# Kernel optimization log

Hardware: AMD Instinct MI355X
Metric: run time of the kernel (lower is better)

## Reference

```python
import jax, jax.numpy as jnp
import numpy as np

B, N, F, H, D, HID = 32, 256, 8, 8, 8, 512  # batch, stocks, features, heads, head_dim, hidden
NEG_SLOPE = 0.2
NEG_INF = -1e30


def setup_inputs() -> dict:
    key = jax.random.key(0)
    ks = jax.random.split(key, 20)
    feat = jax.random.normal(ks[0], (B, F, N), jnp.float32)
    adjs = [(jax.random.uniform(ks[1 + i], (B, N, N)) < 0.05).astype(jnp.float32) for i in range(3)]
    inputs = jnp.concatenate(adjs + [feat], axis=1)  # (B, 3N+F, N)
    s = 0.02  # xavier-ish gain used in the torch init
    stdv = 1.0 / np.sqrt(H * D)
    return {
        'inputs': inputs,
        'W_gat': jax.random.normal(ks[4], (3, HID, H * D), jnp.float32) * stdv,
        'Wu': jax.random.normal(ks[5], (3, H, D, 1), jnp.float32),
        'Wv': jax.random.normal(ks[6], (3, H, D, 1), jnp.float32),
        'b_gat': jax.random.normal(ks[7], (3, H * D), jnp.float32) * stdv,
        'projW': jax.random.normal(ks[8], (3, HID, H * D), jnp.float32) * s,
        'projB': jnp.zeros((3, H * D), jnp.float32),
        'w_self1': jax.random.normal(ks[9], (F, HID), jnp.float32) * s,
        'b_self1': jnp.zeros((HID,), jnp.float32),
        'w_mlp': jax.random.normal(ks[10], (3, H * D, HID), jnp.float32) * s,
        'b_mlp': jnp.zeros((3, HID), jnp.float32),
        'w_self2': jax.random.normal(ks[11], (HID, HID), jnp.float32) * s,
        'b_self2': jnp.zeros((HID,), jnp.float32),
        'sem_w1': jax.random.normal(ks[12], (HID, HID), jnp.float32) * s,
        'sem_b1': jnp.zeros((HID,), jnp.float32),
        'sem_w2': jax.random.normal(ks[13], (HID, 1), jnp.float32) * s,
        'gen_w': jax.random.normal(ks[14], (N * HID, N), jnp.float32) * s,
        'gen_b': jnp.zeros((N,), jnp.float32),
    }


def _mhgat(x, adj, W, Wu, Wv, b, pW, pB):
    # x: (B,N,HID), adj: (B,N,N)
    # rows of adj that are entirely zero are replaced by 1e-6 everywhere
    adj = jnp.where(jnp.all(adj == 0, axis=-1, keepdims=True), 1e-6, adj)
    sup = (x @ W).reshape(B, N, H, D).transpose(0, 2, 1, 3)  # (B,H,N,D)
    f1 = jnp.einsum('bhnd,hd->bhn', sup, Wu[..., 0])[:, :, None, :]  # (B,H,1,N)
    f2 = jnp.einsum('bhnd,hd->bhn', sup, Wv[..., 0])[:, :, :, None]  # (B,H,N,1)
    w = jax.nn.leaky_relu(f1 + f2, NEG_SLOPE)  # (B,H,N,N)
    mw = jnp.einsum('bhij,bjk->bhik', w, adj)  # matmul masking, as in torch source
    mask = mw != 0
    # torch.sparse.softmax: softmax over nonzero entries only, zeros elsewhere
    attn = jax.nn.softmax(jnp.where(mask, mw, NEG_INF), axis=3)
    attn = jnp.where(mask, attn, 0.0)
    out = (attn @ sup).transpose(0, 2, 1, 3).reshape(B, N, H * D) + b
    out = out + x @ pW + pB  # residual projection
    return jnp.tanh(out)


def reference(inputs, W_gat, Wu, Wv, b_gat, projW, projB, w_self1, b_self1,
              w_mlp, b_mlp, w_self2, b_self2, sem_w1, sem_b1, sem_w2, gen_w, gen_b):
    ind_adj = inputs[:, :N, :]
    pos_adj = inputs[:, N:2 * N, :]
    neg_adj = inputs[:, 2 * N:3 * N, :]
    x = inputs[:, 3 * N:, :].transpose(0, 2, 1)  # (B,N,F)
    support = x @ w_self1 + b_self1  # (B,N,HID)
    gat_out = [_mhgat(support, a, W_gat[i], Wu[i], Wv[i], b_gat[i], projW[i], projB[i])
               for i, a in enumerate([ind_adj, pos_adj, neg_adj])]
    ind_s, pos_s, neg_s = gat_out
    s2 = support @ w_self2 + b_self2
    ind_o = ind_s @ w_mlp[0] + b_mlp[0]
    pos_o = neg_s @ w_mlp[1] + b_mlp[1]  # NOTE: bug in original source preserved (uses neg_support)
    neg_o = neg_s @ w_mlp[2] + b_mlp[2]
    emb = jnp.stack([s2, ind_o, pos_o, neg_o], axis=1)  # (B,4,N,HID)
    # semantic fusion attention
    wsem = jnp.tanh(emb @ sem_w1 + sem_b1) @ sem_w2  # (B,4,N,1)
    beta = jax.nn.softmax(wsem, axis=1)
    fused = (beta * emb).sum(axis=1)  # (B,N,HID)
    # PairNorm PN-SI, scale=1
    xc = fused - fused.mean(axis=1, keepdims=True)
    xc = xc / jnp.sqrt(1e-6 + (xc ** 2).sum(axis=2, keepdims=True))
    # generator
    flat = xc.reshape(B, N * HID)
    return jax.nn.sigmoid(flat @ gen_w + gen_b)  # (B,N)
```

## Files before the change

### kernel.cpp

```cpp
#include <hip/hip_runtime.h>
#include <math.h>

#define Bk   32
#define Nk   256
#define Fk   8
#define Hk   8
#define Dk   8
#define HIDk 512
#define HDk  64
#define NROWk 776
#define CAPk 96

typedef __attribute__((ext_vector_type(8))) short short8;
typedef __attribute__((ext_vector_type(4))) float f32x4;

__device__ __forceinline__ float lrelu(float x){ return fmaxf(x, 0.2f*x); }

__device__ __forceinline__ unsigned short f2bf(float x){
  unsigned int u = __float_as_uint(x);
  unsigned int r = (u + 0x7fffu + ((u>>16)&1u)) >> 16;
  return (unsigned short)r;
}

__global__ void k_support(const float* __restrict__ inp, const float* __restrict__ w1,
                          const float* __restrict__ b1, float* __restrict__ support){
  int bn = blockIdx.x; int b = bn >> 8; int n = bn & 255;
  const float* xin = inp + (size_t)b*NROWk*Nk + (size_t)(3*Nk)*Nk + n;
  float x[8];
#pragma unroll
  for (int f=0; f<8; f++) x[f] = xin[(size_t)f*Nk];
  int t = threadIdx.x;
  for (int c = t; c < HIDk; c += 256){
    float s = b1[c];
#pragma unroll
    for (int f=0; f<8; f++) s += x[f]*w1[f*HIDk + c];
    support[(size_t)bn*HIDk + c] = s;
  }
}

__global__ void k_sup(const float* __restrict__ support, const float* __restrict__ W,
                      float* __restrict__ sup){
  __shared__ float srow[4][HIDk+1];
  int b = blockIdx.x >> 6; int n0 = (blockIdx.x & 63) << 2;
  int t = threadIdx.x;
  for (int i = t; i < 4*HIDk; i += 256)
    srow[i>>9][i&511] = support[((size_t)b*Nk + n0 + (i>>9))*HIDk + (i&511)];
  __syncthreads();
  int nl = t >> 6, hd = t & 63;
  const float* srw = srow[nl];
  float s = 0.f;
  for (int c=0;c<HIDk;c++) s += srw[c]*W[c*HDk + hd];
  int h = hd >> 3, d = hd & 7;
  sup[(((size_t)b*Hk + h)*Nk + (n0+nl))*Dk + d] = s;
}

__global__ void k_fuv(const float* __restrict__ sup, const float* __restrict__ Wu,
                      const float* __restrict__ Wv, float* __restrict__ fu, float* __restrict__ fv){
  int i = blockIdx.x*256 + threadIdx.x;
  int h = (i >> 8) & 7;
  const float* s = sup + (size_t)i*Dk;
  float a=0.f, v=0.f;
#pragma unroll
  for (int d=0; d<8; d++){ float sv = s[d]; a += sv*Wu[h*8+d]; v += sv*Wv[h*8+d]; }
  fu[i] = a; fv[i] = v;
}

__global__ void k_rowzero(const float* __restrict__ inp, int rowOff,
                          int* __restrict__ z_cnt, int* __restrict__ z_idx){
  int b = blockIdx.x >> 8, j = blockIdx.x & 255;
  float v = inp[(size_t)b*NROWk*Nk + (size_t)(rowOff+j)*Nk + threadIdx.x];
  __shared__ int flag;
  if (threadIdx.x==0) flag = 0;
  __syncthreads();
  if (v != 0.0f) atomicOr(&flag, 1);
  __syncthreads();
  if (threadIdx.x==0 && flag==0){ int idx = atomicAdd(&z_cnt[b], 1); z_idx[b*Nk + idx] = j; }
}

__global__ void k_csc(const float* __restrict__ inp, int rowOff,
                      int* __restrict__ col_cnt, int* __restrict__ row_idx){
  int b = blockIdx.x >> 8, k = blockIdx.x & 255;
  int j = threadIdx.x;
  __shared__ unsigned char nzf[Nk];
  nzf[j] = (inp[(size_t)b*NROWk*Nk + (size_t)(rowOff+j)*Nk + k] != 0.0f) ? 1 : 0;
  __syncthreads();
  if (j == 0){
    int c = 0; int base = (b*Nk + k)*CAPk;
    for (int jj=0; jj<Nk; jj++) if (nzf[jj]){ if (c < CAPk) row_idx[base + c] = jj; c++; }
    col_cnt[b*Nk + k] = (c > CAPk) ? CAPk : c;
  }
}

__global__ void k_zsum(const float* __restrict__ fu, const float* __restrict__ fv,
                       const int* __restrict__ z_cnt, const int* __restrict__ z_idx,
                       float* __restrict__ zsum){
  int i = blockIdx.x*256 + threadIdx.x;
  int bh = i >> 8; int b = bh >> 3;
  int zc = z_cnt[b];
  float fvi = fv[i], s = 0.f;
  for (int t=0; t<zc; t++){ float x = fvi + fu[(bh<<8) + z_idx[b*Nk+t]]; s += lrelu(x); }
  zsum[i] = s;
}

__global__ __launch_bounds__(256) void k_attn(const float* __restrict__ sup,
    const float* __restrict__ fu_g, const float* __restrict__ fv_g,
    const float* __restrict__ zsum_g, const int* __restrict__ z_cnt,
    const int* __restrict__ col_cnt, const int* __restrict__ row_idx,
    float* __restrict__ ao){
  __shared__ float fu_s[Nk];
  __shared__ float fvt[32];
  __shared__ float zs[32];
  __shared__ float sup_s[Nk*Dk];
  __shared__ float mw[32][Nk+1];
  __shared__ unsigned char maskk[Nk];
  int blk = blockIdx.x;
  int bh = blk >> 3;
  int b  = bh >> 3;
  int h  = bh & 7;
  int i0 = (blk & 7) << 5;
  int t = threadIdx.x;
  fu_s[t] = fu_g[(bh<<8) + t];
  if (t < 32){ fvt[t] = fv_g[(bh<<8) + i0 + t]; zs[t] = zsum_g[(bh<<8) + i0 + t]; }
  for (int i = t; i < Nk*Dk; i += 256) sup_s[i] = sup[(size_t)bh*Nk*Dk + i];
  int zc = z_cnt[b];
  int cnt = col_cnt[b*Nk + t];
  maskk[t] = (cnt > 0 || zc > 0) ? 1 : 0;
  __syncthreads();
  {
    float acc[32];
#pragma unroll
    for (int i=0;i<32;i++) acc[i]=0.f;
    const int* ridx = row_idx + (size_t)(b*Nk + t)*CAPk;
    for (int s=0;s<cnt;s++){
      float fuj = fu_s[ridx[s]];
#pragma unroll
      for (int i=0;i<32;i++){ float x = fvt[i] + fuj; acc[i] += fmaxf(x, 0.2f*x); }
    }
#pragma unroll
    for (int i=0;i<32;i++) mw[i][t] = acc[i] + 1e-6f*zs[i];
  }
  __syncthreads();
  int wv = t>>6, lane = t&63;
  for (int i = wv; i < 32; i += 4){
    float vals[4]; float m = -1e30f;
#pragma unroll
    for (int q=0;q<4;q++){ int kk = lane + (q<<6); float v = mw[i][kk]; vals[q]=v; if (maskk[kk]) m = fmaxf(m, v); }
#pragma unroll
    for (int s=32;s>0;s>>=1) m = fmaxf(m, __shfl_xor(m, s));
    float e[4]; float sum=0.f;
#pragma unroll
    for (int q=0;q<4;q++){ int kk = lane + (q<<6); float p = maskk[kk] ? expf(vals[q]-m) : 0.f; e[q]=p; sum+=p; }
#pragma unroll
    for (int s=32;s>0;s>>=1) sum += __shfl_xor(sum, s);
    float inv = (sum > 0.f) ? 1.f/sum : 0.f;
#pragma unroll
    for (int q=0;q<4;q++){ int kk = lane + (q<<6); mw[i][kk] = e[q]*inv; }
  }
  __syncthreads();
  int il = t>>3, d = t&7;
  float s = 0.f;
  for (int kk=0; kk<Nk; kk++) s += mw[il][kk]*sup_s[kk*Dk + d];
  ao[((size_t)b*Nk + i0 + il)*HDk + (h<<3) + d] = s;
}

__global__ void k_gatout(const float* __restrict__ ao, const float* __restrict__ support,
                         const float* __restrict__ pW, const float* __restrict__ pB,
                         const float* __restrict__ bg, float* __restrict__ gat){
  __shared__ float srow[4][HIDk+1];
  int b = blockIdx.x >> 6; int n0 = (blockIdx.x & 63) << 2;
  int t = threadIdx.x;
  for (int i = t; i < 4*HIDk; i += 256)
    srow[i>>9][i&511] = support[((size_t)b*Nk + n0 + (i>>9))*HIDk + (i&511)];
  __syncthreads();
  int nl = t >> 6, hd = t & 63;
  const float* srw = srow[nl];
  float s = pB[hd] + bg[hd];
  for (int c=0;c<HIDk;c++) s += srw[c]*pW[c*HDk + hd];
  size_t idx = ((size_t)b*Nk + n0 + nl)*HDk + hd;
  gat[idx] = tanhf(s + ao[idx]);
}

__global__ void k_prepT(const float* __restrict__ w_self2, const float* __restrict__ sem_w1,
                        unsigned short* __restrict__ w2T, unsigned short* __restrict__ w1T){
  __shared__ float tile[64][65];
  const float* src = blockIdx.y ? sem_w1 : w_self2;
  unsigned short* dst = blockIdx.y ? w1T : w2T;
  int tk = (blockIdx.x >> 3) << 6;
  int tn = (blockIdx.x & 7) << 6;
  int t = threadIdx.x;
  for (int i = t; i < 64*64; i += 256){
    int r = i >> 6, c = i & 63;
    tile[r][c] = src[(size_t)(tk + r)*HIDk + tn + c];
  }
  __syncthreads();
  for (int i = t; i < 64*64; i += 256){
    int r = i >> 6, c = i & 63;
    dst[(size_t)(tn + r)*HIDk + tk + c] = f2bf(tile[c][r]);
  }
}

template<int MODE>
__global__ __launch_bounds__(256) void k_gemm512(
    const float* __restrict__ A, const unsigned short* __restrict__ BT,
    const float* __restrict__ bias, const float* __restrict__ w2,
    float* __restrict__ outf){
  constexpr int NF = 8;
  constexpr int NPB = NF*16;
  __shared__ uint4 As4[64*4];
  __shared__ uint4 Bs4[NPB*4];
  int row0 = blockIdx.x << 6;
  int col0 = blockIdx.y * NPB;
  int t = threadIdx.x;
  int w = t >> 6, l = t & 63;
  f32x4 acc[NF];
#pragma unroll
  for (int i=0;i<NF;i++) acc[i] = (f32x4){0.f,0.f,0.f,0.f};

  int lrA = t >> 2;
  int slot = t & 3;
  const float* aptr = A + (size_t)(row0 + lrA)*HIDk + slot*8;
  const unsigned short* bbase = BT + (size_t)(col0 + lrA)*HIDk + slot*8;

  float4 av0 = *(const float4*)(aptr);
  float4 av1 = *(const float4*)(aptr + 4);
  uint4 bv0  = *(const uint4*)(bbase);
  uint4 bv1  = *(const uint4*)(bbase + (size_t)64*HIDk);

  for (int kc = 0; kc < 512; kc += 32){
    uint4 apk;
    unsigned short* ap = (unsigned short*)&apk;
    ap[0]=f2bf(av0.x); ap[1]=f2bf(av0.y); ap[2]=f2bf(av0.z); ap[3]=f2bf(av0.w);
    ap[4]=f2bf(av1.x); ap[5]=f2bf(av1.y); ap[6]=f2bf(av1.z); ap[7]=f2bf(av1.w);
    __syncthreads();
    As4[(lrA<<2) + (slot ^ ((lrA>>1)&3))] = apk;
    Bs4[(lrA<<2) + (slot ^ ((lrA>>1)&3))] = bv0;
    {
      int ln = 64 + lrA;
      Bs4[(ln<<2) + (slot ^ ((ln>>1)&3))] = bv1;
    }
    __syncthreads();
    if (kc + 32 < 512){
      av0 = *(const float4*)(aptr + kc + 32);
      av1 = *(const float4*)(aptr + kc + 36);
      bv0 = *(const uint4*)(bbase + kc + 32);
      bv1 = *(const uint4*)(bbase + (size_t)64*HIDk + kc + 32);
    }
    int aRow = (w<<4) + (l&15);
    int ks = l>>4;
    short8 af = *(const short8*)&As4[(aRow<<2) + (ks ^ ((aRow>>1)&3))];
#pragma unroll
    for (int nf = 0; nf < NF; nf++){
      int bRow = (nf<<4) + (l&15);
      short8 bfr = *(const short8*)&Bs4[(bRow<<2) + (ks ^ ((bRow>>1)&3))];
      acc[nf] = __builtin_amdgcn_mfma_f32_16x16x32_bf16(af, bfr, acc[nf], 0, 0, 0);
    }
  }
  int colB = l & 15, rg = l >> 4;
  if (MODE == 0){
#pragma unroll
    for (int nf = 0; nf < NF; nf++){
      int col = col0 + (nf<<4) + colB;
      float bb = bias[col];
#pragma unroll
      for (int r = 0; r < 4; r++){
        int m = row0 + (w<<4) + (rg<<2) + r;
        int mo = ((m>>8)<<10) + (m&255);
        outf[(size_t)mo*HIDk + col] = acc[nf][r] + bb;
      }
    }
  } else {
    float s0=0.f, s1=0.f, s2v=0.f, s3=0.f;
#pragma unroll
    for (int nf = 0; nf < NF; nf++){
      int col = col0 + (nf<<4) + colB;
      float bb = bias[col], wv = w2[col];
      s0  += tanhf(acc[nf][0]+bb)*wv;
      s1  += tanhf(acc[nf][1]+bb)*wv;
      s2v += tanhf(acc[nf][2]+bb)*wv;
      s3  += tanhf(acc[nf][3]+bb)*wv;
    }
#pragma unroll
    for (int mk = 1; mk < 16; mk <<= 1){
      s0  += __shfl_xor(s0, mk);  s1 += __shfl_xor(s1, mk);
      s2v += __shfl_xor(s2v, mk); s3 += __shfl_xor(s3, mk);
    }
    if (colB == 0){
      int m = row0 + (w<<4) + (rg<<2);
      atomicAdd(&outf[m+0], s0);
      atomicAdd(&outf[m+1], s1);
      atomicAdd(&outf[m+2], s2v);
      atomicAdd(&outf[m+3], s3);
    }
  }
}

__global__ void k_mlp(const float* __restrict__ gat, const float* __restrict__ W,
                      const float* __restrict__ bias, float* __restrict__ emb, int chan){
  __shared__ float g[8][HDk];
  int b = blockIdx.x >> 5; int n0 = (blockIdx.x & 31) << 3;
  int t = threadIdx.x;
  for (int i=t;i<8*HDk;i+=256) g[i>>6][i&63] = gat[((size_t)b*Nk + n0 + (i>>6))*HDk + (i&63)];
  __syncthreads();
  for (int pass=0;pass<2;pass++){
    int o = t + (pass<<8);
    float acc[8]={0,0,0,0,0,0,0,0};
    for (int c=0;c<HDk;c++){
      float wv = W[c*HIDk+o];
#pragma unroll
      for (int r=0;r<8;r++) acc[r] += g[r][c]*wv;
    }
    float bs = bias[o];
#pragma unroll
    for (int r=0;r<8;r++) emb[(((size_t)b*4 + chan)*Nk + n0+r)*HIDk + o] = acc[r]+bs;
  }
}

__global__ void k_fused(const float* __restrict__ emb, const float* __restrict__ wsem,
                        float* __restrict__ fused){
  int bn = blockIdx.x; int b = bn>>8, n = bn&255;
  float w0 = wsem[((b<<2)+0)*Nk+n], w1 = wsem[((b<<2)+1)*Nk+n];
  float w2 = wsem[((b<<2)+2)*Nk+n], w3 = wsem[((b<<2)+3)*Nk+n];
  float m = fmaxf(fmaxf(w0,w1),fmaxf(w2,w3));
  float e0=expf(w0-m),e1=expf(w1-m),e2=expf(w2-m),e3=expf(w3-m);
  float inv = 1.f/(e0+e1+e2+e3);
  e0*=inv; e1*=inv; e2*=inv; e3*=inv;
  const float* e = emb + (((size_t)(b<<2))*Nk + n)*HIDk;
  size_t cs = (size_t)Nk*HIDk;
  for (int o = threadIdx.x; o < HIDk; o += 128)
    fused[(size_t)bn*HIDk + o] = e0*e[o] + e1*e[o+cs] + e2*e[o+2*cs] + e3*e[o+3*cs];
}

__global__ void k_cmean(const float* __restrict__ fused, float* __restrict__ cmean){
  int b = blockIdx.x >> 1; int o = ((blockIdx.x & 1) << 8) + threadIdx.x;
  float s=0.f;
  for (int n=0;n<Nk;n++) s += fused[((size_t)b*Nk+n)*HIDk + o];
  cmean[b*HIDk+o] = s*(1.f/Nk);
}

__global__ void k_norm(const float* __restrict__ fused, const float* __restrict__ cmean,
                       float* __restrict__ xc){
  __shared__ float red[4];
  int bn = blockIdx.x; int b = bn>>8;
  int t = threadIdx.x;
  float v0 = fused[(size_t)bn*HIDk + t]       - cmean[b*HIDk + t];
  float v1 = fused[(size_t)bn*HIDk + t+256]   - cmean[b*HIDk + t+256];
  float ss = v0*v0 + v1*v1;
#pragma unroll
  for (int s=32;s>0;s>>=1) ss += __shfl_xor(ss, s);
  if ((t&63)==0) red[t>>6] = ss;
  __syncthreads();
  float tot = red[0]+red[1]+red[2]+red[3];
  float inv = 1.0f/sqrtf(1e-6f + tot);
  xc[(size_t)bn*HIDk + t]     = v0*inv;
  xc[(size_t)bn*HIDk + t+256] = v1*inv;
}

__global__ __launch_bounds__(256) void k_gen(const float* __restrict__ xc, const float* __restrict__ genw,
                                             float* __restrict__ part){
  __shared__ float xs[Bk*HIDk];
  int n = blockIdx.x; int t = threadIdx.x;
  for (int i=t; i<Bk*HIDk; i+=256) xs[i] = xc[((size_t)(i>>9)*Nk + n)*HIDk + (i&511)];
  __syncthreads();
  float acc[32];
#pragma unroll
  for (int b=0;b<32;b++) acc[b]=0.f;
  const float* wp = genw + (size_t)n*HIDk*Nk + t;
  for (int c=0;c<HIDk;c++){
    float wv = wp[(size_t)c*Nk];
#pragma unroll
    for (int b=0;b<32;b++) acc[b] += xs[(b<<9)+c]*wv;
  }
#pragma unroll
  for (int b=0;b<32;b++) part[((size_t)n*Bk + b)*Nk + t] = acc[b];
}

__global__ void k_final(const float* __restrict__ part, const float* __restrict__ genb,
                        float* __restrict__ out){
  int b = blockIdx.x, g = threadIdx.x;
  float s = genb[g];
  for (int n=0;n<Nk;n++) s += part[((size_t)n*Bk + b)*Nk + g];
  out[b*Nk + g] = 1.f/(1.f + expf(-s));
}

extern "C" void kernel_launch(void* const* d_in, const int* in_sizes, int n_in,
                              void* d_out, int out_size, void* d_ws, size_t ws_size,
                              hipStream_t stream){
  const float* inp    = (const float*)d_in[0];
  const float* W_gat  = (const float*)d_in[1];
  const float* Wu     = (const float*)d_in[2];
  const float* Wv     = (const float*)d_in[3];
  const float* b_gat  = (const float*)d_in[4];
  const float* projW  = (const float*)d_in[5];
  const float* projB  = (const float*)d_in[6];
  const float* w_self1= (const float*)d_in[7];
  const float* b_self1= (const float*)d_in[8];
  const float* w_mlp  = (const float*)d_in[9];
  const float* b_mlp  = (const float*)d_in[10];
  const float* w_self2= (const float*)d_in[11];
  const float* b_self2= (const float*)d_in[12];
  const float* sem_w1 = (const float*)d_in[13];
  const float* sem_b1 = (const float*)d_in[14];
  const float* sem_w2 = (const float*)d_in[15];
  const float* gen_w  = (const float*)d_in[16];
  const float* gen_b  = (const float*)d_in[17];
  float* out = (float*)d_out;
  (void)in_sizes; (void)n_in; (void)out_size; (void)ws_size;

  float* w = (float*)d_ws;
  size_t off = 0;
  auto A = [&](size_t n){ float* p = w + off; off += (n + 63) & ~(size_t)63; return p; };
  float* support = A((size_t)Bk*Nk*HIDk);
  float* emb     = A((size_t)Bk*4*Nk*HIDk);
  float* sup0 = A((size_t)Bk*Hk*Nk*Dk); float* sup1 = A((size_t)Bk*Hk*Nk*Dk);
  float* fu0  = A(Bk*Hk*Nk); float* fu1 = A(Bk*Hk*Nk);
  float* fv0  = A(Bk*Hk*Nk); float* fv1 = A(Bk*Hk*Nk);
  float* zs0  = A(Bk*Hk*Nk); float* zs1 = A(Bk*Hk*Nk);
  float* ao0  = A((size_t)Bk*Nk*HDk); float* ao1 = A((size_t)Bk*Nk*HDk);
  float* wsem = A(Bk*4*Nk);
  float* fused= A((size_t)Bk*Nk*HIDk);
  float* cmean= A(Bk*HIDk);
  float* part = A((size_t)Nk*Bk*Nk);
  float* tbuf = A(2*HIDk*HIDk/2);
  unsigned short* w2T = (unsigned short*)tbuf;
  unsigned short* w1T = w2T + HIDk*HIDk;
  int* ib  = (int*)(w + off);
  int* zc0 = ib;              int* zc1 = zc0 + Bk;
  int* zi0 = zc1 + Bk;        int* zi1 = zi0 + Bk*Nk;
  int* cc0 = zi1 + Bk*Nk;     int* cc1 = cc0 + Bk*Nk;
  int* ri0 = cc1 + Bk*Nk;     int* ri1 = ri0 + (size_t)Bk*Nk*CAPk;

  hipMemsetAsync(zc0, 0, 2*Bk*sizeof(int), stream);
  hipMemsetAsync(wsem, 0, (size_t)Bk*4*Nk*sizeof(float), stream);
  k_prepT<<<dim3(64,2), 256, 0, stream>>>(w_self2, sem_w1, w2T, w1T);
  k_support<<<Bk*Nk, 256, 0, stream>>>(inp, w_self1, b_self1, support);
  k_sup<<<Bk*(Nk/4), 256, 0, stream>>>(support, W_gat, sup0);
  k_sup<<<Bk*(Nk/4), 256, 0, stream>>>(support, W_gat + 2*HIDk*HDk, sup1);
  k_fuv<<<Bk*Hk*Nk/256, 256, 0, stream>>>(sup0, Wu, Wv, fu0, fv0);
  k_fuv<<<Bk*Hk*Nk/256, 256, 0, stream>>>(sup1, Wu + 2*Hk*Dk, Wv + 2*Hk*Dk, fu1, fv1);
  k_rowzero<<<Bk*Nk, 256, 0, stream>>>(inp, 0,    zc0, zi0);
  k_rowzero<<<Bk*Nk, 256, 0, stream>>>(inp, 2*Nk, zc1, zi1);
  k_csc<<<Bk*Nk, 256, 0, stream>>>(inp, 0,    cc0, ri0);
  k_csc<<<Bk*Nk, 256, 0, stream>>>(inp, 2*Nk, cc1, ri1);
  k_zsum<<<Bk*Hk*Nk/256, 256, 0, stream>>>(fu0, fv0, zc0, zi0, zs0);
  k_zsum<<<Bk*Hk*Nk/256, 256, 0, stream>>>(fu1, fv1, zc1, zi1, zs1);
  k_attn<<<Bk*Hk*(Nk/32), 256, 0, stream>>>(sup0, fu0, fv0, zs0, zc0, cc0, ri0, ao0);
  k_attn<<<Bk*Hk*(Nk/32), 256, 0, stream>>>(sup1, fu1, fv1, zs1, zc1, cc1, ri1, ao1);
  k_gatout<<<Bk*(Nk/4), 256, 0, stream>>>(ao0, support, projW,                projB,         b_gat,         ao0);
  k_gatout<<<Bk*(Nk/4), 256, 0, stream>>>(ao1, support, projW + 2*HIDk*HDk,   projB + 2*HDk, b_gat + 2*HDk, ao1);
  k_gemm512<0><<<dim3(128,4), 256, 0, stream>>>(support, w2T, b_self2, nullptr, emb);
  k_mlp<<<Bk*(Nk/8), 256, 0, stream>>>(ao0, w_mlp,               b_mlp,          emb, 1);
  k_mlp<<<Bk*(Nk/8), 256, 0, stream>>>(ao1, w_mlp + HDk*HIDk,    b_mlp + HIDk,   emb, 2);
  k_mlp<<<Bk*(Nk/8), 256, 0, stream>>>(ao1, w_mlp + 2*HDk*HIDk,  b_mlp + 2*HIDk, emb, 3);
  k_gemm512<1><<<dim3(512,4), 256, 0, stream>>>(emb, w1T, sem_b1, sem_w2, wsem);
  k_fused<<<Bk*Nk, 128, 0, stream>>>(emb, wsem, fused);
  k_cmean<<<Bk*2, 256, 0, stream>>>(fused, cmean);
  k_norm<<<Bk*Nk, 256, 0, stream>>>(fused, cmean, fused);
  k_gen<<<Nk, 256, 0, stream>>>(fused, gen_w, part);
  k_final<<<Bk, 256, 0, stream>>>(part, gen_b, out);
}
```

Before: 891.9 us.

## Split generator GEMV over hidden slices and read activations directly

```diff
diff --git a/kernel.cpp b/kernel.cpp
--- a/kernel.cpp
+++ b/kernel.cpp
@@ -10,6 +10,7 @@
 #define HDk  64
 #define NROWk 776
 #define CAPk 96
+#define GSLICE 4
 
 typedef __attribute__((ext_vector_type(8))) short short8;
 typedef __attribute__((ext_vector_type(4))) float f32x4;
@@ -357,28 +358,40 @@
 
 __global__ __launch_bounds__(256) void k_gen(const float* __restrict__ xc, const float* __restrict__ genw,
                                              float* __restrict__ part){
-  __shared__ float xs[Bk*HIDk];
-  int n = blockIdx.x; int t = threadIdx.x;
-  for (int i=t; i<Bk*HIDk; i+=256) xs[i] = xc[((size_t)(i>>9)*Nk + n)*HIDk + (i&511)];
-  __syncthreads();
+  int n = blockIdx.x, q = blockIdx.y;
+  int t = threadIdx.x;
+  int c0 = q << 7;
   float acc[32];
 #pragma unroll
   for (int b=0;b<32;b++) acc[b]=0.f;
-  const float* wp = genw + (size_t)n*HIDk*Nk + t;
-  for (int c=0;c<HIDk;c++){
-    float wv = wp[(size_t)c*Nk];
-#pragma unroll
-    for (int b=0;b<32;b++) acc[b] += xs[(b<<9)+c]*wv;
-  }
-#pragma unroll
-  for (int b=0;b<32;b++) part[((size_t)n*Bk + b)*Nk + t] = acc[b];
+  const float* wp = genw + ((size_t)n*HIDk + c0)*Nk + t;
+  for (int c = 0; c < 128; c += 4){
+    float w0 = wp[(size_t)(c+0)*Nk];
+    float w1 = wp[(size_t)(c+1)*Nk];
+    float w2 = wp[(size_t)(c+2)*Nk];
+    float w3 = wp[(size_t)(c+3)*Nk];
+#pragma unroll
+    for (int b = 0; b < 32; b++){
+      const float4 xv = *(const float4*)(xc + ((size_t)b*Nk + n)*HIDk + c0 + c);
+      acc[b] = fmaf(xv.x, w0, fmaf(xv.y, w1, fmaf(xv.z, w2, fmaf(xv.w, w3, acc[b]))));
+    }
+  }
+#pragma unroll
+  for (int b=0;b<32;b++) part[((size_t)b*(Nk*GSLICE) + (n<<2) + q)*Nk + t] = acc[b];
 }
 
 __global__ void k_final(const float* __restrict__ part, const float* __restrict__ genb,
                         float* __restrict__ out){
   int b = blockIdx.x, g = threadIdx.x;
-  float s = genb[g];
-  for (int n=0;n<Nk;n++) s += part[((size_t)n*Bk + b)*Nk + g];
+  float s0=0.f, s1=0.f, s2=0.f, s3=0.f;
+  const float* p = part + (size_t)b*(Nk*GSLICE)*Nk + g;
+  for (int s = 0; s < Nk*GSLICE; s += 4){
+    s0 += p[(size_t)(s+0)*Nk];
+    s1 += p[(size_t)(s+1)*Nk];
+    s2 += p[(size_t)(s+2)*Nk];
+    s3 += p[(size_t)(s+3)*Nk];
+  }
+  float s = genb[g] + s0+s1+s2+s3;
   out[b*Nk + g] = 1.f/(1.f + expf(-s));
 }
 
@@ -419,7 +432,7 @@
   float* wsem = A(Bk*4*Nk);
   float* fused= A((size_t)Bk*Nk*HIDk);
   float* cmean= A(Bk*HIDk);
-  float* part = A((size_t)Nk*Bk*Nk);
+  float* part = A((size_t)Bk*Nk*GSLICE*Nk);
   float* tbuf = A(2*HIDk*HIDk/2);
   unsigned short* w2T = (unsigned short*)tbuf;
   unsigned short* w1T = w2T + HIDk*HIDk;
@@ -455,6 +468,6 @@
   k_fused<<<Bk*Nk, 128, 0, stream>>>(emb, wsem, fused);
   k_cmean<<<Bk*2, 256, 0, stream>>>(fused, cmean);
   k_norm<<<Bk*Nk, 256, 0, stream>>>(fused, cmean, fused);
-  k_gen<<<Nk, 256, 0, stream>>>(fused, gen_w, part);
+  k_gen<<<dim3(Nk, GSLICE), 256, 0, stream>>>(fused, gen_w, part);
   k_final<<<Bk, 256, 0, stream>>>(part, gen_b, out);
 }
```

New measurement: 949.2 us. 6.4% more time.
